# Performance work log

Measured on AMD Instinct MI355X. Metric: run time of the kernel, lower is better.

The kernel has to match this reference:

```python
import jax, jax.numpy as jnp
import numpy as np

N_NODES = 50000
N_EDGES = 1600000
NFEAT, NHID, NCLASS = 512, 128, 40


def setup_inputs() -> dict:
    key = jax.random.key(0)
    ks = jax.random.split(key, 10)
    x = jax.random.normal(ks[0], (N_NODES, NFEAT), dtype=jnp.float32)
    edge_src = jax.random.randint(ks[1], (N_EDGES,), 0, N_NODES, dtype=jnp.int32)
    edge_dst = jax.random.randint(ks[2], (N_EDGES,), 0, N_NODES, dtype=jnp.int32)
    edge_weight = jax.random.uniform(ks[3], (N_EDGES,), dtype=jnp.float32)
    # GraphConvolution params: gc1 (nfeat->nhid), one additional (nhid->nhid), gc2 (nhid->nclass)
    s1 = 1.0 / np.sqrt(NHID)
    s2 = 1.0 / np.sqrt(NCLASS)
    W1 = jax.random.uniform(ks[4], (NFEAT, NHID), minval=-s1, maxval=s1, dtype=jnp.float32)
    b1 = jax.random.uniform(ks[5], (NHID,), minval=-s1, maxval=s1, dtype=jnp.float32)
    Wh = jax.random.uniform(ks[6], (NHID, NHID), minval=-s1, maxval=s1, dtype=jnp.float32)
    bh = jax.random.uniform(ks[7], (NHID,), minval=-s1, maxval=s1, dtype=jnp.float32)
    W2 = jax.random.uniform(ks[8], (NHID, NCLASS), minval=-s2, maxval=s2, dtype=jnp.float32)
    b2 = jax.random.uniform(ks[9], (NCLASS,), minval=-s2, maxval=s2, dtype=jnp.float32)
    return {"x": x, "edge_src": edge_src, "edge_dst": edge_dst, "edge_weight": edge_weight,
            "W1": W1, "b1": b1, "Wh": Wh, "bh": bh, "W2": W2, "b2": b2}


def reference(x, edge_src, edge_dst, edge_weight, W1, b1, Wh, bh, W2, b2):
    def spmm(h):
        # out[i] = sum_j adj[i, j] * h[j]  with adj given as weighted edge list (src=j, dst=i)
        return jax.ops.segment_sum(edge_weight[:, None] * h[edge_src], edge_dst,
                                   num_segments=x.shape[0])

    def gconv(h, W, b):
        return spmm(h @ W) + b  # dense transform then sparse aggregation

    h = jax.nn.relu(gconv(x, W1, b1))       # gc1
    h = jax.nn.relu(gconv(h, Wh, bh))        # additional hidden layer
    h = gconv(h, W2, b2)                     # gc2
    return jax.nn.log_softmax(h, axis=1)
```

## Files before the change

### kernel.cpp

```cpp
#include <hip/hip_runtime.h>
#include <hip/hip_bf16.h>
#include <math.h>

#define N_NODES 50000
#define N_EDGES 1600000
#define NFEAT 512
#define NHID 128
#define NCLASS 40

#define NBUCKETS 196
#define BUCKET_CAP 16384

typedef __attribute__((ext_vector_type(8))) short bf16x8;
typedef __attribute__((ext_vector_type(4))) float f32x4;

static __device__ __forceinline__ float asfloat_u32(unsigned int u) {
    union { unsigned int u; float f; } c;
    c.u = u;
    return c.f;
}
static __device__ __forceinline__ unsigned int asu32_f(float f) {
    union { float f; unsigned int u; } c;
    c.f = f;
    return c.u;
}
static __device__ __forceinline__ unsigned short f2bf(float f) {
    union { float f; unsigned int u; } c;
    c.f = f;
    unsigned int r = c.u + 0x7FFFu + ((c.u >> 16) & 1u);
    return (unsigned short)(r >> 16);
}

__global__ __launch_bounds__(256) void prep_kernel(const float* __restrict__ W1,
                                                   unsigned short* __restrict__ Wt1,
                                                   const float* __restrict__ Wh,
                                                   unsigned short* __restrict__ Wth,
                                                   const float* __restrict__ W2,
                                                   unsigned short* __restrict__ Wt2,
                                                   int* __restrict__ bucketCursor) {
    int idx = blockIdx.x * 256 + threadIdx.x;
    if (idx < NFEAT * NHID) {
        int k = idx >> 7;
        int n = idx & 127;
        Wt1[(size_t)n * NFEAT + k] = f2bf(W1[idx]);
    } else if (idx < NFEAT * NHID + NHID * NHID) {
        int j = idx - NFEAT * NHID;
        int k = j >> 7;
        int n = j & 127;
        Wth[(size_t)n * NHID + k] = f2bf(Wh[j]);
    } else if (idx < NFEAT * NHID + NHID * NHID + 64 * NHID) {
        int j = idx - (NFEAT * NHID + NHID * NHID);
        int n = j & 63;
        int k = j >> 6;
        Wt2[(size_t)n * NHID + k] = (n < NCLASS) ? f2bf(W2[(size_t)k * NCLASS + n]) : 0;
    } else {
        int j = idx - (NFEAT * NHID + NHID * NHID + 64 * NHID);
        if (j < NBUCKETS) bucketCursor[j] = j * BUCKET_CAP;
    }
}

#define LDPA 72
#define GEMM_LDS_BYTES ((64 + 128) * LDPA * 2)

template <bool A_IS_BF16>
static __device__ __forceinline__ void gemm64_body(const void* __restrict__ Ap,
                                                   const unsigned short* __restrict__ Wt,
                                                   unsigned short* __restrict__ C,
                                                   const int M, const int K,
                                                   char* smem, int bid) {
    unsigned short* As = (unsigned short*)smem;
    unsigned short* Bs = (unsigned short*)smem + 64 * LDPA;
    const int tid = threadIdx.x;
    const int wave = tid >> 6;
    const int lane = tid & 63;
    const int ln = lane & 15;
    const int quad = lane >> 4;
    const int row0 = bid * 64;

    const int ar = tid >> 2;
    const int ac = (tid & 3) * 16;
    const bool arOk = (row0 + ar) < M;
    const int bn = tid >> 1;
    const int bk = (tid & 1) * 32;

    f32x4 acc[8];
#pragma unroll
    for (int t = 0; t < 8; ++t) acc[t] = (f32x4){0.f, 0.f, 0.f, 0.f};

    for (int kc = 0; kc < K; kc += 64) {
        bf16x8 va0, va1;
        if (A_IS_BF16) {
            if (arOk) {
                const unsigned short* Ab =
                    (const unsigned short*)Ap + (size_t)(row0 + ar) * K + kc + ac;
                va0 = *(const bf16x8*)Ab;
                va1 = *(const bf16x8*)(Ab + 8);
            } else {
#pragma unroll
                for (int i = 0; i < 8; ++i) { va0[i] = 0; va1[i] = 0; }
            }
        } else {
            if (arOk) {
                const float* Af = (const float*)Ap + (size_t)(row0 + ar) * K + kc + ac;
                float4 f0 = *(const float4*)(Af);
                float4 f1 = *(const float4*)(Af + 4);
                float4 f2 = *(const float4*)(Af + 8);
                float4 f3 = *(const float4*)(Af + 12);
                va0[0] = (short)f2bf(f0.x); va0[1] = (short)f2bf(f0.y);
                va0[2] = (short)f2bf(f0.z); va0[3] = (short)f2bf(f0.w);
                va0[4] = (short)f2bf(f1.x); va0[5] = (short)f2bf(f1.y);
                va0[6] = (short)f2bf(f1.z); va0[7] = (short)f2bf(f1.w);
                va1[0] = (short)f2bf(f2.x); va1[1] = (short)f2bf(f2.y);
                va1[2] = (short)f2bf(f2.z); va1[3] = (short)f2bf(f2.w);
                va1[4] = (short)f2bf(f3.x); va1[5] = (short)f2bf(f3.y);
                va1[6] = (short)f2bf(f3.z); va1[7] = (short)f2bf(f3.w);
            } else {
#pragma unroll
                for (int i = 0; i < 8; ++i) { va0[i] = 0; va1[i] = 0; }
            }
        }
        const unsigned short* Bg = Wt + (size_t)bn * K + kc + bk;
        bf16x8 vb0 = *(const bf16x8*)(Bg);
        bf16x8 vb1 = *(const bf16x8*)(Bg + 8);
        bf16x8 vb2 = *(const bf16x8*)(Bg + 16);
        bf16x8 vb3 = *(const bf16x8*)(Bg + 24);

        __syncthreads();
        *(bf16x8*)&As[ar * LDPA + ac] = va0;
        *(bf16x8*)&As[ar * LDPA + ac + 8] = va1;
        *(bf16x8*)&Bs[bn * LDPA + bk] = vb0;
        *(bf16x8*)&Bs[bn * LDPA + bk + 8] = vb1;
        *(bf16x8*)&Bs[bn * LDPA + bk + 16] = vb2;
        *(bf16x8*)&Bs[bn * LDPA + bk + 24] = vb3;
        __syncthreads();

        bf16x8 a0 = *(const bf16x8*)&As[(wave * 16 + ln) * LDPA + quad * 8];
        bf16x8 a1 = *(const bf16x8*)&As[(wave * 16 + ln) * LDPA + 32 + quad * 8];
#pragma unroll
        for (int t = 0; t < 8; ++t) {
            bf16x8 b0 = *(const bf16x8*)&Bs[(t * 16 + ln) * LDPA + quad * 8];
            acc[t] = __builtin_amdgcn_mfma_f32_16x16x32_bf16(a0, b0, acc[t], 0, 0, 0);
        }
#pragma unroll
        for (int t = 0; t < 8; ++t) {
            bf16x8 b1 = *(const bf16x8*)&Bs[(t * 16 + ln) * LDPA + 32 + quad * 8];
            acc[t] = __builtin_amdgcn_mfma_f32_16x16x32_bf16(a1, b1, acc[t], 0, 0, 0);
        }
    }

#pragma unroll
    for (int t = 0; t < 8; ++t) {
#pragma unroll
        for (int r = 0; r < 4; ++r) {
            int row = row0 + wave * 16 + quad * 4 + r;
            if (row < M) C[(size_t)row * 128 + t * 16 + ln] = f2bf(acc[t][r]);
        }
    }
}

static __device__ __forceinline__ void bin_body(const int* __restrict__ src,
                                                const int* __restrict__ dst,
                                                const float* __restrict__ w,
                                                int* __restrict__ bucketCursor,
                                                uint2* __restrict__ binned,
                                                int n, char* smem, int bid) {
    int* hist = (int*)smem;
    int* cur = (int*)smem + NBUCKETS;
    const int tid = threadIdx.x;
    const int base = bid * 4096;
    if (tid < NBUCKETS) hist[tid] = 0;
    __syncthreads();
#pragma unroll
    for (int r = 0; r < 16; ++r) {
        int e = base + r * 256 + tid;
        if (e < n) atomicAdd(&hist[dst[e] >> 8], 1);
    }
    __syncthreads();
    if (tid < NBUCKETS && hist[tid] > 0)
        cur[tid] = atomicAdd(&bucketCursor[tid], hist[tid]);
    __syncthreads();
#pragma unroll
    for (int r = 0; r < 16; ++r) {
        int e = base + r * 256 + tid;
        if (e < n) {
            int d = dst[e];
            int pos = atomicAdd(&cur[d >> 8], 1);
            uint2 rec;
            rec.x = (unsigned int)src[e] | ((unsigned int)(d & 255) << 16);
            rec.y = asu32_f(w[e]);
            binned[pos] = rec;
        }
    }
}

#define GEMM1_BLOCKS 782
#define BIN_BLOCKS 391
__global__ __launch_bounds__(256) void fused_gemm1_bin(const float* __restrict__ x,
                                                       const unsigned short* __restrict__ Wt1,
                                                       unsigned short* __restrict__ tb,
                                                       const int* __restrict__ src,
                                                       const int* __restrict__ dst,
                                                       const float* __restrict__ w,
                                                       int* __restrict__ bucketCursor,
                                                       uint2* __restrict__ binned) {
    __shared__ char smem[GEMM_LDS_BYTES];
    if (blockIdx.x < GEMM1_BLOCKS) {
        gemm64_body<false>(x, Wt1, tb, N_NODES, NFEAT, smem, blockIdx.x);
    } else {
        bin_body(src, dst, w, bucketCursor, binned, N_EDGES, smem,
                 blockIdx.x - GEMM1_BLOCKS);
    }
}

__global__ __launch_bounds__(256) void gemm64_l2(const unsigned short* __restrict__ A,
                                                 const unsigned short* __restrict__ Wt,
                                                 unsigned short* __restrict__ C) {
    __shared__ char smem[GEMM_LDS_BYTES];
    gemm64_body<true>(A, Wt, C, N_NODES, NHID, smem, blockIdx.x);
}

__global__ __launch_bounds__(1024) void build_csr(const uint2* __restrict__ binned,
                                                  const int* __restrict__ bucketCursor,
                                                  unsigned int* __restrict__ pairs,
                                                  int* __restrict__ row_ptr) {
    __shared__ int bs[256];
    __shared__ int hist[256];
    __shared__ int sc[256];
    __shared__ int cur[256];
    const int b = blockIdx.x;
    const int tid = threadIdx.x;

    if (tid < 256) bs[tid] = (tid < NBUCKETS) ? (bucketCursor[tid] - tid * BUCKET_CAP) : 0;
    if (tid < 256) hist[tid] = 0;
    __syncthreads();
    for (int off = 1; off < 256; off <<= 1) {
        int t = 0;
        if (tid < 256 && tid >= off) t = bs[tid - off];
        __syncthreads();
        if (tid < 256) bs[tid] += t;
        __syncthreads();
    }
    const int cnt = bucketCursor[b] - b * BUCKET_CAP;
    const int segStart = bs[b] - cnt;
    if (b == NBUCKETS - 1 && tid == 0) row_ptr[N_NODES] = bs[NBUCKETS - 1];
    const uint2* seg = binned + (size_t)b * BUCKET_CAP;

    for (int i = tid; i < cnt; i += 1024)
        atomicAdd(&hist[seg[i].x >> 16], 1);
    __syncthreads();
    if (tid < 256) {
        int v = hist[tid];
        sc[tid] = v;
    }
    __syncthreads();
    for (int off = 1; off < 256; off <<= 1) {
        int t = 0;
        if (tid < 256 && tid >= off) t = sc[tid - off];
        __syncthreads();
        if (tid < 256) sc[tid] += t;
        __syncthreads();
    }
    if (tid < 256) {
        int excl = sc[tid] - hist[tid];
        int node = b * 256 + tid;
        if (node < N_NODES) row_ptr[node] = segStart + excl;
        cur[tid] = segStart + excl;
    }
    __syncthreads();
    for (int i = tid; i < cnt; i += 1024) {
        uint2 p = seg[i];
        int pos = atomicAdd(&cur[p.x >> 16], 1);
        pairs[pos] = (p.x & 0xFFFFu) | ((unsigned int)f2bf(asfloat_u32(p.y)) << 16);
    }
}

#define LDP2 136
__global__ __launch_bounds__(256) void gemm_n48(const unsigned short* __restrict__ A,
                                                const unsigned short* __restrict__ Wt2,
                                                unsigned short* __restrict__ C, int M) {
    __shared__ unsigned short As[64 * LDP2];
    __shared__ unsigned short Bs[48 * LDP2];
    const int tid = threadIdx.x;
    const int wave = tid >> 6;
    const int lane = tid & 63;
    const int ln = lane & 15;
    const int quad = lane >> 4;
    const int row0 = blockIdx.x * 64;

#pragma unroll
    for (int i = 0; i < 4; ++i) {
        int q = tid + 256 * i;
        int r = q >> 4;
        int c = (q & 15) * 8;
        bf16x8 v;
        if (row0 + r < M) {
            v = *(const bf16x8*)(A + (size_t)(row0 + r) * 128 + c);
        } else {
#pragma unroll
            for (int j = 0; j < 8; ++j) v[j] = 0;
        }
        *(bf16x8*)&As[r * LDP2 + c] = v;
    }
#pragma unroll
    for (int i = 0; i < 3; ++i) {
        int q = tid + 256 * i;
        int r = q >> 4;
        int c = (q & 15) * 8;
        *(bf16x8*)&Bs[r * LDP2 + c] = *(const bf16x8*)(Wt2 + (size_t)r * 128 + c);
    }
    __syncthreads();

    f32x4 acc[3];
#pragma unroll
    for (int t = 0; t < 3; ++t) acc[t] = (f32x4){0.f, 0.f, 0.f, 0.f};

#pragma unroll
    for (int kc = 0; kc < 128; kc += 32) {
        bf16x8 a = *(const bf16x8*)&As[(wave * 16 + ln) * LDP2 + kc + quad * 8];
#pragma unroll
        for (int t = 0; t < 3; ++t) {
            bf16x8 b = *(const bf16x8*)&Bs[(t * 16 + ln) * LDP2 + kc + quad * 8];
            acc[t] = __builtin_amdgcn_mfma_f32_16x16x32_bf16(a, b, acc[t], 0, 0, 0);
        }
    }

#pragma unroll
    for (int t = 0; t < 3; ++t) {
        int col = t * 16 + ln;
        if (col < NCLASS) {
#pragma unroll
            for (int r = 0; r < 4; ++r) {
                int row = row0 + wave * 16 + quad * 4 + r;
                if (row < M) C[(size_t)row * NCLASS + col] = f2bf(acc[t][r]);
            }
        }
    }
}

__global__ __launch_bounds__(256) void spmm_bias_relu_bf16(const unsigned short* __restrict__ t,
                                                           const int* __restrict__ row_ptr,
                                                           const unsigned int* __restrict__ pairs,
                                                           const float* __restrict__ bias,
                                                           unsigned short* __restrict__ out) {
    const int node = blockIdx.x * 4 + (threadIdx.x >> 6);
    const int lane = threadIdx.x & 63;
    const int g = lane >> 4;
    const int fl = (lane & 15) * 8;
    const int e0 = row_ptr[node];
    const int e1 = row_ptr[node + 1];
    float acc8[8];
#pragma unroll
    for (int j = 0; j < 8; ++j) acc8[j] = 0.f;

    int e = e0;
    for (; e + 32 <= e1; e += 32) {
        unsigned int p[8];
        uint4 v[8];
#pragma unroll
        for (int i = 0; i < 8; ++i) p[i] = pairs[e + 4 * i + g];
#pragma unroll
        for (int i = 0; i < 8; ++i)
            v[i] = *(const uint4*)(t + (size_t)(p[i] & 0xFFFFu) * 128 + fl);
#pragma unroll
        for (int i = 0; i < 8; ++i) {
            float w = asfloat_u32(p[i] & 0xFFFF0000u);
            acc8[0] += w * asfloat_u32(v[i].x << 16);
            acc8[1] += w * asfloat_u32(v[i].x & 0xFFFF0000u);
            acc8[2] += w * asfloat_u32(v[i].y << 16);
            acc8[3] += w * asfloat_u32(v[i].y & 0xFFFF0000u);
            acc8[4] += w * asfloat_u32(v[i].z << 16);
            acc8[5] += w * asfloat_u32(v[i].z & 0xFFFF0000u);
            acc8[6] += w * asfloat_u32(v[i].w << 16);
            acc8[7] += w * asfloat_u32(v[i].w & 0xFFFF0000u);
        }
    }
    for (; e + 4 <= e1; e += 4) {
        unsigned int p = pairs[e + g];
        uint4 v = *(const uint4*)(t + (size_t)(p & 0xFFFFu) * 128 + fl);
        float w = asfloat_u32(p & 0xFFFF0000u);
        acc8[0] += w * asfloat_u32(v.x << 16);
        acc8[1] += w * asfloat_u32(v.x & 0xFFFF0000u);
        acc8[2] += w * asfloat_u32(v.y << 16);
        acc8[3] += w * asfloat_u32(v.y & 0xFFFF0000u);
        acc8[4] += w * asfloat_u32(v.z << 16);
        acc8[5] += w * asfloat_u32(v.z & 0xFFFF0000u);
        acc8[6] += w * asfloat_u32(v.w << 16);
        acc8[7] += w * asfloat_u32(v.w & 0xFFFF0000u);
    }
    if (g < e1 - e) {
        unsigned int p = pairs[e + g];
        uint4 v = *(const uint4*)(t + (size_t)(p & 0xFFFFu) * 128 + fl);
        float w = asfloat_u32(p & 0xFFFF0000u);
        acc8[0] += w * asfloat_u32(v.x << 16);
        acc8[1] += w * asfloat_u32(v.x & 0xFFFF0000u);
        acc8[2] += w * asfloat_u32(v.y << 16);
        acc8[3] += w * asfloat_u32(v.y & 0xFFFF0000u);
        acc8[4] += w * asfloat_u32(v.z << 16);
        acc8[5] += w * asfloat_u32(v.z & 0xFFFF0000u);
        acc8[6] += w * asfloat_u32(v.w << 16);
        acc8[7] += w * asfloat_u32(v.w & 0xFFFF0000u);
    }
#pragma unroll
    for (int j = 0; j < 8; ++j) {
        acc8[j] += __shfl_xor(acc8[j], 16);
        acc8[j] += __shfl_xor(acc8[j], 32);
    }
    if (g == 0) {
        float4 b0 = *(const float4*)&bias[fl];
        float4 b1 = *(const float4*)&bias[fl + 4];
        acc8[0] = fmaxf(acc8[0] + b0.x, 0.f);
        acc8[1] = fmaxf(acc8[1] + b0.y, 0.f);
        acc8[2] = fmaxf(acc8[2] + b0.z, 0.f);
        acc8[3] = fmaxf(acc8[3] + b0.w, 0.f);
        acc8[4] = fmaxf(acc8[4] + b1.x, 0.f);
        acc8[5] = fmaxf(acc8[5] + b1.y, 0.f);
        acc8[6] = fmaxf(acc8[6] + b1.z, 0.f);
        acc8[7] = fmaxf(acc8[7] + b1.w, 0.f);
        uint4 o;
        o.x = ((unsigned int)f2bf(acc8[0])) | (((unsigned int)f2bf(acc8[1])) << 16);
        o.y = ((unsigned int)f2bf(acc8[2])) | (((unsigned int)f2bf(acc8[3])) << 16);
        o.z = ((unsigned int)f2bf(acc8[4])) | (((unsigned int)f2bf(acc8[5])) << 16);
        o.w = ((unsigned int)f2bf(acc8[6])) | (((unsigned int)f2bf(acc8[7])) << 16);
        *(uint4*)(out + (size_t)node * 128 + fl) = o;
    }
}

__global__ __launch_bounds__(256) void spmm_logsoftmax(const unsigned short* __restrict__ t,
                                                       const int* __restrict__ row_ptr,
                                                       const unsigned int* __restrict__ pairs,
                                                       const float* __restrict__ bias,
                                                       float* __restrict__ out) {
    const int node = blockIdx.x * 4 + (threadIdx.x >> 6);
    const int lane = threadIdx.x & 63;
    const int e0 = row_ptr[node];
    const int e1 = row_ptr[node + 1];
    const bool act = lane < NCLASS;
    float acc = 0.f;
    int e = e0;
    for (; e + 8 <= e1; e += 8) {
        unsigned int p[8];
#pragma unroll
        for (int i = 0; i < 8; ++i) p[i] = pairs[e + i];
        if (act) {
            float v[8];
#pragma unroll
            for (int i = 0; i < 8; ++i)
                v[i] = asfloat_u32((unsigned int)t[(size_t)(p[i] & 0xFFFFu) * NCLASS + lane] << 16);
#pragma unroll
            for (int i = 0; i < 8; ++i) acc += asfloat_u32(p[i] & 0xFFFF0000u) * v[i];
        }
    }
    for (; e < e1; ++e) {
        unsigned int p = pairs[e];
        if (act)
            acc += asfloat_u32(p & 0xFFFF0000u) *
                   asfloat_u32((unsigned int)t[(size_t)(p & 0xFFFFu) * NCLASS + lane] << 16);
    }
    float logit = act ? (acc + bias[lane]) : -INFINITY;
    float m = logit;
#pragma unroll
    for (int off = 32; off; off >>= 1) m = fmaxf(m, __shfl_xor(m, off));
    float ex = act ? __expf(logit - m) : 0.f;
    float ssum = ex;
#pragma unroll
    for (int off = 32; off; off >>= 1) ssum += __shfl_xor(ssum, off);
    if (act) out[(size_t)node * NCLASS + lane] = logit - m - __logf(ssum);
}


extern "C" void kernel_launch(void* const* d_in, const int* in_sizes, int n_in,
                              void* d_out, int out_size, void* d_ws, size_t ws_size,
                              hipStream_t stream) {
    const float* x = (const float*)d_in[0];
    const int* edge_src = (const int*)d_in[1];
    const int* edge_dst = (const int*)d_in[2];
    const float* edge_weight = (const float*)d_in[3];
    const float* W1 = (const float*)d_in[4];
    const float* b1 = (const float*)d_in[5];
    const float* Wh = (const float*)d_in[6];
    const float* bh = (const float*)d_in[7];
    const float* W2 = (const float*)d_in[8];
    const float* b2 = (const float*)d_in[9];
    float* out = (float*)d_out;

    size_t off = 0;
    auto carve = [&](size_t bytes) {
        void* p = (char*)d_ws + off;
        off += (bytes + 511) & ~(size_t)511;
        return p;
    };
    unsigned short* tb = (unsigned short*)carve((size_t)N_NODES * 128 * 2);
    unsigned short* hb = (unsigned short*)carve((size_t)N_NODES * 128 * 2);
    unsigned short* t3 = (unsigned short*)carve((size_t)N_NODES * NCLASS * 2);
    unsigned short* Wt1 = (unsigned short*)carve((size_t)NFEAT * NHID * 2);
    unsigned short* Wth = (unsigned short*)carve((size_t)NHID * NHID * 2);
    unsigned short* Wt2 = (unsigned short*)carve((size_t)64 * NHID * 2);
    int* row_ptr = (int*)carve((size_t)(N_NODES + 4) * 4);
    int* bucketCursor = (int*)carve((size_t)NBUCKETS * 4);
    uint2* binned = (uint2*)carve((size_t)NBUCKETS * BUCKET_CAP * 8);
    unsigned int* pairs = (unsigned int*)carve((size_t)N_EDGES * 4);
    (void)ws_size; (void)n_in; (void)in_sizes; (void)out_size;

    const int prepBlocks =
        (NFEAT * NHID + NHID * NHID + 64 * NHID + NBUCKETS + 255) / 256;
    const int spmmBlocks = N_NODES / 4;
    const int gemmBlocks = (N_NODES + 63) / 64;

    prep_kernel<<<prepBlocks, 256, 0, stream>>>(W1, Wt1, Wh, Wth, W2, Wt2, bucketCursor);

    fused_gemm1_bin<<<GEMM1_BLOCKS + BIN_BLOCKS, 256, 0, stream>>>(
        x, Wt1, tb, edge_src, edge_dst, edge_weight, bucketCursor, binned);

    build_csr<<<NBUCKETS, 1024, 0, stream>>>(binned, bucketCursor, pairs, row_ptr);

    spmm_bias_relu_bf16<<<spmmBlocks, 256, 0, stream>>>(tb, row_ptr, pairs, b1, hb);

    gemm64_l2<<<gemmBlocks, 256, 0, stream>>>(hb, Wth, tb);
    spmm_bias_relu_bf16<<<spmmBlocks, 256, 0, stream>>>(tb, row_ptr, pairs, bh, hb);

    gemm_n48<<<gemmBlocks, 256, 0, stream>>>(hb, Wt2, t3, N_NODES);
    spmm_logsoftmax<<<spmmBlocks, 256, 0, stream>>>(t3, row_ptr, pairs, b2, out);
}
```

Before: 389.6 us.

## Double-buffer GEMM B tiles, stage binning in LDS, pad layer-3 features to 64

The shared GEMM body now loads A fragments straight from global memory into registers and double-buffers the B tile in LDS, prefetching the next K-chunk so only one barrier per iteration remains. The edge-binning step first scatters records into an LDS staging area using a local prefix scan, then copies each bucket to global memory contiguously, replacing scattered global writes. The final GEMM writes a 64-wide padded output so the last SpMM can use vectorized 8-byte gathers with 16 lanes per edge across 4 edges at a time, plus a 16-lane log-softmax. These changes raise LDS use and add scan barriers in exchange for fewer global scatter writes and better gather coalescing.

```diff
diff --git a/kernel.cpp b/kernel.cpp
--- a/kernel.cpp
+++ b/kernel.cpp
@@ -59,8 +59,8 @@
     }
 }
 
-#define LDPA 72
-#define GEMM_LDS_BYTES ((64 + 128) * LDPA * 2)
+#define LDPB 72
+#define GEMM_LDS_BYTES (2 * 128 * LDPB * 2)
 
 template <bool A_IS_BF16>
 static __device__ __forceinline__ void gemm64_body(const void* __restrict__ Ap,
@@ -68,8 +68,8 @@
                                                    unsigned short* __restrict__ C,
                                                    const int M, const int K,
                                                    char* smem, int bid) {
-    unsigned short* As = (unsigned short*)smem;
-    unsigned short* Bs = (unsigned short*)smem + 64 * LDPA;
+    unsigned short* Bs0 = (unsigned short*)smem;
+    unsigned short* Bs1 = (unsigned short*)smem + 128 * LDPB;
     const int tid = threadIdx.x;
     const int wave = tid >> 6;
     const int lane = tid & 63;
@@ -77,76 +77,115 @@
     const int quad = lane >> 4;
     const int row0 = bid * 64;
 
-    const int ar = tid >> 2;
-    const int ac = (tid & 3) * 16;
-    const bool arOk = (row0 + ar) < M;
+    const int arow = row0 + wave * 16 + ln;
+    const bool aOk = arow < M;
+    const unsigned short* Abf = (const unsigned short*)Ap + (size_t)arow * K + quad * 8;
+    const float* Af = (const float*)Ap + (size_t)arow * K + quad * 8;
+
     const int bn = tid >> 1;
     const int bk = (tid & 1) * 32;
+    const unsigned short* Bg = Wt + (size_t)bn * K + bk;
+
+    const int NK = K >> 6;
 
     f32x4 acc[8];
 #pragma unroll
     for (int t = 0; t < 8; ++t) acc[t] = (f32x4){0.f, 0.f, 0.f, 0.f};
 
-    for (int kc = 0; kc < K; kc += 64) {
-        bf16x8 va0, va1;
+    bf16x8 qb0, qb1, qb2, qb3;
+    bf16x8 pva0, pva1;
+    float4 pf0, pf1, pf2, pf3;
+
+#define GV2_LOAD_A(kc)                                                       \
+    do {                                                                     \
+        if (A_IS_BF16) {                                                     \
+            if (aOk) {                                                       \
+                pva0 = *(const bf16x8*)(Abf + (kc));                         \
+                pva1 = *(const bf16x8*)(Abf + (kc) + 32);                    \
+            }                                                                \
+        } else {                                                             \
+            if (aOk) {                                                       \
+                pf0 = *(const float4*)(Af + (kc));                           \
+                pf1 = *(const float4*)(Af + (kc) + 4);                       \
+                pf2 = *(const float4*)(Af + (kc) + 32);                      \
+                pf3 = *(const float4*)(Af + (kc) + 36);                      \
+            }                                                                \
+        }                                                                    \
+    } while (0)
+
+#define GV2_LOAD_B(kc)                                                       \
+    do {                                                                     \
+        qb0 = *(const bf16x8*)(Bg + (kc));                                   \
+        qb1 = *(const bf16x8*)(Bg + (kc) + 8);                               \
+        qb2 = *(const bf16x8*)(Bg + (kc) + 16);                              \
+        qb3 = *(const bf16x8*)(Bg + (kc) + 24);                              \
+    } while (0)
+
+#define GV2_STORE_B(Bdst)                                                    \
+    do {                                                                     \
+        *(bf16x8*)&(Bdst)[bn * LDPB + bk] = qb0;                             \
+        *(bf16x8*)&(Bdst)[bn * LDPB + bk + 8] = qb1;                         \
+        *(bf16x8*)&(Bdst)[bn * LDPB + bk + 16] = qb2;                        \
+        *(bf16x8*)&(Bdst)[bn * LDPB + bk + 24] = qb3;                        \
+    } while (0)
+
+    GV2_LOAD_B(0);
+    GV2_STORE_B(Bs0);
+    GV2_LOAD_A(0);
+    if (NK > 1) GV2_LOAD_B(64);
+    __syncthreads();
+
+    for (int i = 0; i < NK; ++i) {
+        unsigned short* Bcur = (i & 1) ? Bs1 : Bs0;
+        unsigned short* Bnxt = (i & 1) ? Bs0 : Bs1;
+
+        bf16x8 a0, a1;
         if (A_IS_BF16) {
-            if (arOk) {
-                const unsigned short* Ab =
-                    (const unsigned short*)Ap + (size_t)(row0 + ar) * K + kc + ac;
-                va0 = *(const bf16x8*)Ab;
-                va1 = *(const bf16x8*)(Ab + 8);
+            if (aOk) {
+                a0 = pva0;
+                a1 = pva1;
             } else {
 #pragma unroll
-                for (int i = 0; i < 8; ++i) { va0[i] = 0; va1[i] = 0; }
+                for (int j = 0; j < 8; ++j) { a0[j] = 0; a1[j] = 0; }
             }
         } else {
-            if (arOk) {
-                const float* Af = (const float*)Ap + (size_t)(row0 + ar) * K + kc + ac;
-                float4 f0 = *(const float4*)(Af);
-                float4 f1 = *(const float4*)(Af + 4);
-                float4 f2 = *(const float4*)(Af + 8);
-                float4 f3 = *(const float4*)(Af + 12);
-                va0[0] = (short)f2bf(f0.x); va0[1] = (short)f2bf(f0.y);
-                va0[2] = (short)f2bf(f0.z); va0[3] = (short)f2bf(f0.w);
-                va0[4] = (short)f2bf(f1.x); va0[5] = (short)f2bf(f1.y);
-                va0[6] = (short)f2bf(f1.z); va0[7] = (short)f2bf(f1.w);
-                va1[0] = (short)f2bf(f2.x); va1[1] = (short)f2bf(f2.y);
-                va1[2] = (short)f2bf(f2.z); va1[3] = (short)f2bf(f2.w);
-                va1[4] = (short)f2bf(f3.x); va1[5] = (short)f2bf(f3.y);
-                va1[6] = (short)f2bf(f3.z); va1[7] = (short)f2bf(f3.w);
+            if (aOk) {
+                a0[0] = (short)f2bf(pf0.x); a0[1] = (short)f2bf(pf0.y);
+                a0[2] = (short)f2bf(pf0.z); a0[3] = (short)f2bf(pf0.w);
+                a0[4] = (short)f2bf(pf1.x); a0[5] = (short)f2bf(pf1.y);
+                a0[6] = (short)f2bf(pf1.z); a0[7] = (short)f2bf(pf1.w);
+                a1[0] = (short)f2bf(pf2.x); a1[1] = (short)f2bf(pf2.y);
+                a1[2] = (short)f2bf(pf2.z); a1[3] = (short)f2bf(pf2.w);
+                a1[4] = (short)f2bf(pf3.x); a1[5] = (short)f2bf(pf3.y);
+                a1[6] = (short)f2bf(pf3.z); a1[7] = (short)f2bf(pf3.w);
             } else {
 #pragma unroll
-                for (int i = 0; i < 8; ++i) { va0[i] = 0; va1[i] = 0; }
+                for (int j = 0; j < 8; ++j) { a0[j] = 0; a1[j] = 0; }
             }
         }
-        const unsigned short* Bg = Wt + (size_t)bn * K + kc + bk;
-        bf16x8 vb0 = *(const bf16x8*)(Bg);
-        bf16x8 vb1 = *(const bf16x8*)(Bg + 8);
-        bf16x8 vb2 = *(const bf16x8*)(Bg + 16);
-        bf16x8 vb3 = *(const bf16x8*)(Bg + 24);
-
+        if (i + 1 < NK) GV2_LOAD_A((i + 1) * 64);
+
+#pragma unroll
+        for (int t = 0; t < 8; ++t) {
+            bf16x8 b0 = *(const bf16x8*)&Bcur[(t * 16 + ln) * LDPB + quad * 8];
+            acc[t] = __builtin_amdgcn_mfma_f32_16x16x32_bf16(a0, b0, acc[t], 0, 0, 0);
+        }
+#pragma unroll
+        for (int t = 0; t < 8; ++t) {
+            bf16x8 b1 = *(const bf16x8*)&Bcur[(t * 16 + ln) * LDPB + 32 + quad * 8];
+            acc[t] = __builtin_amdgcn_mfma_f32_16x16x32_bf16(a1, b1, acc[t], 0, 0, 0);
+        }
+
+        if (i + 1 < NK) {
+            GV2_STORE_B(Bnxt);
+            if (i + 2 < NK) GV2_LOAD_B((i + 2) * 64);
+        }
         __syncthreads();
-        *(bf16x8*)&As[ar * LDPA + ac] = va0;
-        *(bf16x8*)&As[ar * LDPA + ac + 8] = va1;
-        *(bf16x8*)&Bs[bn * LDPA + bk] = vb0;
-        *(bf16x8*)&Bs[bn * LDPA + bk + 8] = vb1;
-        *(bf16x8*)&Bs[bn * LDPA + bk + 16] = vb2;
-        *(bf16x8*)&Bs[bn * LDPA + bk + 24] = vb3;
-        __syncthreads();
-
-        bf16x8 a0 = *(const bf16x8*)&As[(wave * 16 + ln) * LDPA + quad * 8];
-        bf16x8 a1 = *(const bf16x8*)&As[(wave * 16 + ln) * LDPA + 32 + quad * 8];
-#pragma unroll
-        for (int t = 0; t < 8; ++t) {
-            bf16x8 b0 = *(const bf16x8*)&Bs[(t * 16 + ln) * LDPA + quad * 8];
-            acc[t] = __builtin_amdgcn_mfma_f32_16x16x32_bf16(a0, b0, acc[t], 0, 0, 0);
-        }
-#pragma unroll
-        for (int t = 0; t < 8; ++t) {
-            bf16x8 b1 = *(const bf16x8*)&Bs[(t * 16 + ln) * LDPA + 32 + quad * 8];
-            acc[t] = __builtin_amdgcn_mfma_f32_16x16x32_bf16(a1, b1, acc[t], 0, 0, 0);
-        }
-    }
+    }
+
+#undef GV2_LOAD_A
+#undef GV2_LOAD_B
+#undef GV2_STORE_B
 
 #pragma unroll
     for (int t = 0; t < 8; ++t) {
@@ -164,11 +203,17 @@
                                                 int* __restrict__ bucketCursor,
                                                 uint2* __restrict__ binned,
                                                 int n, char* smem, int bid) {
-    int* hist = (int*)smem;
-    int* cur = (int*)smem + NBUCKETS;
+    uint2* recs = (uint2*)smem;
+    int* hist = (int*)(smem + 32768);
+    int* lincl = hist + 256;
+    int* gbase = lincl + 256;
+    int* cur = gbase + 256;
     const int tid = threadIdx.x;
+    const int wave = tid >> 6;
+    const int lane = tid & 63;
     const int base = bid * 4096;
-    if (tid < NBUCKETS) hist[tid] = 0;
+
+    hist[tid] = 0;
     __syncthreads();
 #pragma unroll
     for (int r = 0; r < 16; ++r) {
@@ -176,8 +221,17 @@
         if (e < n) atomicAdd(&hist[dst[e] >> 8], 1);
     }
     __syncthreads();
-    if (tid < NBUCKETS && hist[tid] > 0)
-        cur[tid] = atomicAdd(&bucketCursor[tid], hist[tid]);
+    int v = hist[tid];
+    lincl[tid] = v;
+    __syncthreads();
+    for (int off = 1; off < 256; off <<= 1) {
+        int t = (tid >= off) ? lincl[tid - off] : 0;
+        __syncthreads();
+        lincl[tid] += t;
+        __syncthreads();
+    }
+    if (tid < NBUCKETS && v > 0) gbase[tid] = atomicAdd(&bucketCursor[tid], v);
+    cur[tid] = lincl[tid] - v;
     __syncthreads();
 #pragma unroll
     for (int r = 0; r < 16; ++r) {
@@ -188,8 +242,16 @@
             uint2 rec;
             rec.x = (unsigned int)src[e] | ((unsigned int)(d & 255) << 16);
             rec.y = asu32_f(w[e]);
-            binned[pos] = rec;
-        }
+            recs[pos] = rec;
+        }
+    }
+    __syncthreads();
+    for (int B = wave; B < NBUCKETS; B += 4) {
+        int cnt = hist[B];
+        if (cnt == 0) continue;
+        int lst = lincl[B] - cnt;
+        int g = gbase[B];
+        for (int i = lane; i < cnt; i += 64) binned[g + i] = recs[lst + i];
     }
 }
 
@@ -275,11 +337,11 @@
 }
 
 #define LDP2 136
-__global__ __launch_bounds__(256) void gemm_n48(const unsigned short* __restrict__ A,
+__global__ __launch_bounds__(256) void gemm_n64(const unsigned short* __restrict__ A,
                                                 const unsigned short* __restrict__ Wt2,
                                                 unsigned short* __restrict__ C, int M) {
     __shared__ unsigned short As[64 * LDP2];
-    __shared__ unsigned short Bs[48 * LDP2];
+    __shared__ unsigned short Bs[64 * LDP2];
     const int tid = threadIdx.x;
     const int wave = tid >> 6;
     const int lane = tid & 63;
@@ -302,7 +364,7 @@
         *(bf16x8*)&As[r * LDP2 + c] = v;
     }
 #pragma unroll
-    for (int i = 0; i < 3; ++i) {
+    for (int i = 0; i < 4; ++i) {
         int q = tid + 256 * i;
         int r = q >> 4;
         int c = (q & 15) * 8;
@@ -310,29 +372,26 @@
     }
     __syncthreads();
 
-    f32x4 acc[3];
-#pragma unroll
-    for (int t = 0; t < 3; ++t) acc[t] = (f32x4){0.f, 0.f, 0.f, 0.f};
+    f32x4 acc[4];
+#pragma unroll
+    for (int t = 0; t < 4; ++t) acc[t] = (f32x4){0.f, 0.f, 0.f, 0.f};
 
 #pragma unroll
     for (int kc = 0; kc < 128; kc += 32) {
         bf16x8 a = *(const bf16x8*)&As[(wave * 16 + ln) * LDP2 + kc + quad * 8];
 #pragma unroll
-        for (int t = 0; t < 3; ++t) {
+        for (int t = 0; t < 4; ++t) {
             bf16x8 b = *(const bf16x8*)&Bs[(t * 16 + ln) * LDP2 + kc + quad * 8];
             acc[t] = __builtin_amdgcn_mfma_f32_16x16x32_bf16(a, b, acc[t], 0, 0, 0);
         }
     }
 
 #pragma unroll
-    for (int t = 0; t < 3; ++t) {
-        int col = t * 16 + ln;
-        if (col < NCLASS) {
-#pragma unroll
-            for (int r = 0; r < 4; ++r) {
-                int row = row0 + wave * 16 + quad * 4 + r;
-                if (row < M) C[(size_t)row * NCLASS + col] = f2bf(acc[t][r]);
-            }
+    for (int t = 0; t < 4; ++t) {
+#pragma unroll
+        for (int r = 0; r < 4; ++r) {
+            int row = row0 + wave * 16 + quad * 4 + r;
+            if (row < M) C[(size_t)row * 64 + t * 16 + ln] = f2bf(acc[t][r]);
         }
     }
 }
@@ -432,39 +491,70 @@
                                                        float* __restrict__ out) {
     const int node = blockIdx.x * 4 + (threadIdx.x >> 6);
     const int lane = threadIdx.x & 63;
+    const int g = lane >> 4;
+    const int fe = (lane & 15) * 4;
     const int e0 = row_ptr[node];
     const int e1 = row_ptr[node + 1];
-    const bool act = lane < NCLASS;
-    float acc = 0.f;
+    float a0 = 0.f, a1 = 0.f, a2 = 0.f, a3 = 0.f;
     int e = e0;
-    for (; e + 8 <= e1; e += 8) {
+    for (; e + 32 <= e1; e += 32) {
         unsigned int p[8];
-#pragma unroll
-        for (int i = 0; i < 8; ++i) p[i] = pairs[e + i];
-        if (act) {
-            float v[8];
-#pragma unroll
-            for (int i = 0; i < 8; ++i)
-                v[i] = asfloat_u32((unsigned int)t[(size_t)(p[i] & 0xFFFFu) * NCLASS + lane] << 16);
-#pragma unroll
-            for (int i = 0; i < 8; ++i) acc += asfloat_u32(p[i] & 0xFFFF0000u) * v[i];
-        }
-    }
-    for (; e < e1; ++e) {
-        unsigned int p = pairs[e];
-        if (act)
-            acc += asfloat_u32(p & 0xFFFF0000u) *
-                   asfloat_u32((unsigned int)t[(size_t)(p & 0xFFFFu) * NCLASS + lane] << 16);
-    }
-    float logit = act ? (acc + bias[lane]) : -INFINITY;
-    float m = logit;
-#pragma unroll
-    for (int off = 32; off; off >>= 1) m = fmaxf(m, __shfl_xor(m, off));
-    float ex = act ? __expf(logit - m) : 0.f;
-    float ssum = ex;
-#pragma unroll
-    for (int off = 32; off; off >>= 1) ssum += __shfl_xor(ssum, off);
-    if (act) out[(size_t)node * NCLASS + lane] = logit - m - __logf(ssum);
+        uint2 v[8];
+#pragma unroll
+        for (int i = 0; i < 8; ++i) p[i] = pairs[e + 4 * i + g];
+#pragma unroll
+        for (int i = 0; i < 8; ++i)
+            v[i] = *(const uint2*)(t + (size_t)(p[i] & 0xFFFFu) * 64 + fe);
+#pragma unroll
+        for (int i = 0; i < 8; ++i) {
+            float w = asfloat_u32(p[i] & 0xFFFF0000u);
+            a0 += w * asfloat_u32(v[i].x << 16);
+            a1 += w * asfloat_u32(v[i].x & 0xFFFF0000u);
+            a2 += w * asfloat_u32(v[i].y << 16);
+            a3 += w * asfloat_u32(v[i].y & 0xFFFF0000u);
+        }
+    }
+    for (; e + 4 <= e1; e += 4) {
+        unsigned int p = pairs[e + g];
+        uint2 v = *(const uint2*)(t + (size_t)(p & 0xFFFFu) * 64 + fe);
+        float w = asfloat_u32(p & 0xFFFF0000u);
+        a0 += w * asfloat_u32(v.x << 16);
+        a1 += w * asfloat_u32(v.x & 0xFFFF0000u);
+        a2 += w * asfloat_u32(v.y << 16);
+        a3 += w * asfloat_u32(v.y & 0xFFFF0000u);
+    }
+    if (g < e1 - e) {
+        unsigned int p = pairs[e + g];
+        uint2 v = *(const uint2*)(t + (size_t)(p & 0xFFFFu) * 64 + fe);
+        float w = asfloat_u32(p & 0xFFFF0000u);
+        a0 += w * asfloat_u32(v.x << 16);
+        a1 += w * asfloat_u32(v.x & 0xFFFF0000u);
+        a2 += w * asfloat_u32(v.y << 16);
+        a3 += w * asfloat_u32(v.y & 0xFFFF0000u);
+    }
+    a0 += __shfl_xor(a0, 16); a0 += __shfl_xor(a0, 32);
+    a1 += __shfl_xor(a1, 16); a1 += __shfl_xor(a1, 32);
+    a2 += __shfl_xor(a2, 16); a2 += __shfl_xor(a2, 32);
+    a3 += __shfl_xor(a3, 16); a3 += __shfl_xor(a3, 32);
+
+    const bool valid = (lane & 15) < 10;
+    float l0 = -INFINITY, l1 = -INFINITY, l2 = -INFINITY, l3 = -INFINITY;
+    if (valid) {
+        float4 b = *(const float4*)&bias[fe];
+        l0 = a0 + b.x; l1 = a1 + b.y; l2 = a2 + b.z; l3 = a3 + b.w;
+    }
+    float m = fmaxf(fmaxf(l0, l1), fmaxf(l2, l3));
+#pragma unroll
+    for (int off = 8; off; off >>= 1) m = fmaxf(m, __shfl_xor(m, off));
+    float s = valid ? (__expf(l0 - m) + __expf(l1 - m) + __expf(l2 - m) + __expf(l3 - m)) : 0.f;
+#pragma unroll
+    for (int off = 8; off; off >>= 1) s += __shfl_xor(s, off);
+    if (valid && g == 0) {
+        float ls = __logf(s);
+        float4 o;
+        o.x = l0 - m - ls; o.y = l1 - m - ls; o.z = l2 - m - ls; o.w = l3 - m - ls;
+        *(float4*)&out[(size_t)node * NCLASS + fe] = o;
+    }
 }
 
 
@@ -491,7 +581,7 @@
     };
     unsigned short* tb = (unsigned short*)carve((size_t)N_NODES * 128 * 2);
     unsigned short* hb = (unsigned short*)carve((size_t)N_NODES * 128 * 2);
-    unsigned short* t3 = (unsigned short*)carve((size_t)N_NODES * NCLASS * 2);
+    unsigned short* t3 = (unsigned short*)carve((size_t)N_NODES * 64 * 2);
     unsigned short* Wt1 = (unsigned short*)carve((size_t)NFEAT * NHID * 2);
     unsigned short* Wth = (unsigned short*)carve((size_t)NHID * NHID * 2);
     unsigned short* Wt2 = (unsigned short*)carve((size_t)64 * NHID * 2);
@@ -518,6 +608,6 @@
     gemm64_l2<<<gemmBlocks, 256, 0, stream>>>(hb, Wth, tb);
     spmm_bias_relu_bf16<<<spmmBlocks, 256, 0, stream>>>(tb, row_ptr, pairs, bh, hb);
 
-    gemm_n48<<<gemmBlocks, 256, 0, stream>>>(hb, Wt2, t3, N_NODES);
+    gemm_n64<<<gemmBlocks, 256, 0, stream>>>(hb, Wt2, t3, N_NODES);
     spmm_logsoftmax<<<spmmBlocks, 256, 0, stream>>>(t3, row_ptr, pairs, b2, out);
 }
```

Result: no change. 386.4 us (-0.8%).
